# Optimization experiments

Hardware: AMD Instinct MI355X
Metric: run time of the kernel (lower is better)

The kernel has to match this reference:

```python
import jax, jax.numpy as jnp
import numpy as np

LN_EPS = 1e-5

def setup_inputs() -> dict:
    key = jax.random.key(0)
    ks = jax.random.split(key, 7)
    B, S, D = 16, 2048, 512
    scale_g = 1.0 / np.sqrt(2 * D)
    scale_c = 1.0 / np.sqrt(2 * D)
    return {
        "points": jax.random.normal(ks[0], (B, S, D), dtype=jnp.float32),
        "W_gate": jax.random.uniform(ks[1], (2 * D, 2 * D), jnp.float32, -scale_g, scale_g),
        "b_gate": jax.random.uniform(ks[2], (2 * D,), jnp.float32, -scale_g, scale_g),
        "W_cand": jax.random.uniform(ks[3], (2 * D, D), jnp.float32, -scale_c, scale_c),
        "b_cand": jax.random.uniform(ks[4], (D,), jnp.float32, -scale_c, scale_c),
        "gamma": jnp.ones((D,), jnp.float32),
        "beta": jnp.zeros((D,), jnp.float32),
    }

def _layer_norm(x, gamma, beta):
    mu = jnp.mean(x, axis=-1, keepdims=True)
    var = jnp.mean(jnp.square(x - mu), axis=-1, keepdims=True)
    return (x - mu) * jax.lax.rsqrt(var + LN_EPS) * gamma + beta

def reference(points, W_gate, b_gate, W_cand, b_cand, gamma, beta):
    B, S, D = points.shape
    h0 = jnp.zeros((B, D), dtype=points.dtype)

    def step(h, p_t):  # p_t: [B, D]
        combined = jnp.concatenate([p_t, h], axis=1)          # [B, 2D]
        gates = combined @ W_gate + b_gate                    # [B, 2D]
        r = jax.nn.sigmoid(gates[:, :D])
        z = jax.nn.sigmoid(gates[:, D:])
        cand_in = jnp.concatenate([p_t, r * h], axis=1)       # [B, 2D]
        c = jnp.tanh(cand_in @ W_cand + b_cand)               # [B, D]
        h_new = (1.0 - z) * h + z * c
        return h_new, h_new

    _, states = jax.lax.scan(step, h0, jnp.swapaxes(points, 0, 1))  # [S, B, D]
    states = jnp.swapaxes(states, 0, 1)                             # [B, S, D]
    displacement = states - points
    deformed = points + displacement
    return _layer_norm(deformed, gamma, beta)
```

## Files before the change

kernel.cpp:

```cpp
#include <hip/hip_runtime.h>


typedef _Float16 half8 __attribute__((ext_vector_type(8)));
typedef _Float16 half4 __attribute__((ext_vector_type(4)));
typedef float floatx4 __attribute__((ext_vector_type(4)));
typedef int int4v __attribute__((ext_vector_type(4)));

#define NBLK 16
#define TPB 256
#define S_LEN 2048

#define SZ_WPK (96ull * 16 * 64 * 8 * 2)
#define OFF_WHPK 0ull
#define OFF_WXPK (OFF_WHPK + SZ_WPK)
#define OFF_HBUF (OFF_WXPK + SZ_WPK)
#define OFF_RH (OFF_HBUF + 32768ull)
#define OFF_XGT (OFF_RH + 32768ull)

__device__ __forceinline__ float sigmoid_f(float x) {
  return 1.f / (1.f + __expf(-x));
}
__device__ __forceinline__ float tanh_f(float x) {
  x = fminf(15.f, fmaxf(-15.f, x));
  float e = __expf(2.f * x);
  return (e - 1.f) / (e + 1.f);
}

__device__ __forceinline__ void ld8_cg(const unsigned* p, int4v (&d)[8]) {
  asm volatile(
      "global_load_dwordx4 %0, %8, off sc0 sc1\n\t"
      "global_load_dwordx4 %1, %8, off offset:16 sc0 sc1\n\t"
      "global_load_dwordx4 %2, %8, off offset:128 sc0 sc1\n\t"
      "global_load_dwordx4 %3, %8, off offset:144 sc0 sc1\n\t"
      "global_load_dwordx4 %4, %8, off offset:256 sc0 sc1\n\t"
      "global_load_dwordx4 %5, %8, off offset:272 sc0 sc1\n\t"
      "global_load_dwordx4 %6, %8, off offset:384 sc0 sc1\n\t"
      "global_load_dwordx4 %7, %8, off offset:400 sc0 sc1\n\t"
      "s_waitcnt vmcnt(0)"
      : "=&v"(d[0]), "=&v"(d[1]), "=&v"(d[2]), "=&v"(d[3]), "=&v"(d[4]),
        "=&v"(d[5]), "=&v"(d[6]), "=&v"(d[7])
      : "v"(p)
      : "memory");
}
__device__ __forceinline__ void st_dw(unsigned* p, unsigned v) {
  asm volatile("global_store_dword %0, %1, off sc0 sc1" ::"v"(p), "v"(v)
               : "memory");
}
__device__ __forceinline__ unsigned pk2(unsigned p1, unsigned p0) {
  return __builtin_amdgcn_perm(p1, p0, 0x05040100u);
}

__device__ __forceinline__ void stage_val(const unsigned* p, unsigned tokhi,
                                          int4v* lds_dst) {
  int4v d[8];
  for (;;) {
    ld8_cg(p, d);
    unsigned acc = 0;
#pragma unroll
    for (int u = 0; u < 8; ++u)
#pragma unroll
      for (int c = 0; c < 4; ++c) acc |= ((unsigned)d[u][c]) ^ tokhi;
    if (__all((int)((acc >> 16) == 0u))) break;
    __builtin_amdgcn_s_sleep(2);
  }
#pragma unroll
  for (int u = 0; u < 4; ++u) {
    int4v f;
    f[0] = (int)pk2((unsigned)d[2 * u][1], (unsigned)d[2 * u][0]);
    f[1] = (int)pk2((unsigned)d[2 * u][3], (unsigned)d[2 * u][2]);
    f[2] = (int)pk2((unsigned)d[2 * u + 1][1], (unsigned)d[2 * u + 1][0]);
    f[3] = (int)pk2((unsigned)d[2 * u + 1][3], (unsigned)d[2 * u + 1][2]);
    lds_dst[u * 64] = f;
  }
}

__global__ void pack_kernel(const float* __restrict__ Wg,
                            const float* __restrict__ Wc,
                            _Float16* __restrict__ Whpk,
                            _Float16* __restrict__ Wxpk) {
  int unit = blockIdx.x * 4 + (threadIdx.x >> 6);
  int lane = threadIdx.x & 63;
  int set = (unit >= 1536) ? 1 : 0;
  int rem = unit - set * 1536;
  int tile = rem >> 4, kc = rem & 15;
  int kb = kc * 32 + ((lane >> 4) << 3);
  int n = lane & 15;
  int row0 = set ? 0 : 512;
  half8 w;
  if (tile < 64) {
    int col = tile * 16 + n;
#pragma unroll
    for (int jj = 0; jj < 8; ++jj)
      w[jj] = (_Float16)Wg[(size_t)(row0 + kb + jj) * 1024 + col];
  } else {
    int col = (tile - 64) * 16 + n;
#pragma unroll
    for (int jj = 0; jj < 8; ++jj)
      w[jj] = (_Float16)Wc[(size_t)(row0 + kb + jj) * 512 + col];
  }
  _Float16* dst = set ? Wxpk : Whpk;
  *(half8*)(dst + ((size_t)rem * 64 + lane) * 8) = w;
}

__global__ __launch_bounds__(TPB) void xgemm_kernel(
    const float* __restrict__ points, const float* __restrict__ b_gate,
    const float* __restrict__ b_cand, const _Float16* __restrict__ Wxpk,
    _Float16* __restrict__ xgt) {
  __shared__ _Float16 x_lds[16][520];
  const int tid = threadIdx.x;
  const int wave = tid >> 6, lane = tid & 63;
  const int ln15 = lane & 15, q = lane >> 4;
  const int t = blockIdx.x;
  const int m = tid & 15, ch = tid >> 4;

  const float* xp = points + ((size_t)m * S_LEN + t) * 512 + ch * 32;
#pragma unroll
  for (int u = 0; u < 4; ++u) {
    float4 f0 = ((const float4*)xp)[2 * u];
    float4 f1 = ((const float4*)xp)[2 * u + 1];
    half8 hv;
    hv[0] = (_Float16)f0.x; hv[1] = (_Float16)f0.y;
    hv[2] = (_Float16)f0.z; hv[3] = (_Float16)f0.w;
    hv[4] = (_Float16)f1.x; hv[5] = (_Float16)f1.y;
    hv[6] = (_Float16)f1.z; hv[7] = (_Float16)f1.w;
    *(half8*)&x_lds[m][ch * 32 + u * 8] = hv;
  }
  __syncthreads();

  for (int tile = wave; tile < 96; tile += 4) {
    const _Float16* W = Wxpk + (size_t)tile * 8192;
    floatx4 a0 = {0.f, 0.f, 0.f, 0.f}, a1 = {0.f, 0.f, 0.f, 0.f};
#pragma unroll
    for (int kc = 0; kc < 16; kc += 2) {
      a0 = __builtin_amdgcn_mfma_f32_16x16x32_f16(
          *(const half8*)&x_lds[ln15][kc * 32 + q * 8],
          *(const half8*)(W + ((size_t)kc * 64 + lane) * 8), a0, 0, 0, 0);
      a1 = __builtin_amdgcn_mfma_f32_16x16x32_f16(
          *(const half8*)&x_lds[ln15][(kc + 1) * 32 + q * 8],
          *(const half8*)(W + ((size_t)(kc + 1) * 64 + lane) * 8), a1, 0, 0, 0);
    }
    float bias = (tile < 64) ? b_gate[tile * 16 + ln15]
                             : b_cand[(tile - 64) * 16 + ln15];
    half4 o;
#pragma unroll
    for (int i = 0; i < 4; ++i) o[i] = (_Float16)(a0[i] + a1[i] + bias);
    *(half4*)(xgt + (((size_t)t * 96 + tile) * 16 + ln15) * 16 + q * 4) = o;
  }
}

__global__ __launch_bounds__(TPB, 1) void rec_kernel(
    const _Float16* __restrict__ Whpk, const _Float16* __restrict__ xgt,
    unsigned* __restrict__ h2, unsigned* __restrict__ rh2,
    float* __restrict__ out) {
  __shared__ int4v hsh[2][1024];
  __shared__ float z_lds[16][36];

  const int tid = threadIdx.x;
  const int wave = tid >> 6, lane = tid & 63;
  const int ln15 = lane & 15, q = lane >> 4;
  const int j = blockIdx.x;

  const int twA = (wave < 2) ? (2 * j + wave) : (32 + 2 * j + (wave - 2));
  const int twB = 64 + 2 * j + (wave & 1);
  const int colA = 32 * j + 16 * (wave & 1) + ln15;

  half8 wA[16], wB[16];
  {
    const _Float16* sA = Whpk + (size_t)twA * 8192 + lane * 8;
#pragma unroll
    for (int kc = 0; kc < 16; ++kc) wA[kc] = *(const half8*)(sA + kc * 512);
  }
  if (wave < 2) {
    const _Float16* sB = Whpk + (size_t)twB * 8192 + lane * 8;
#pragma unroll
    for (int kc = 0; kc < 16; ++kc) wB[kc] = *(const half8*)(sB + kc * 512);
  }

  const unsigned* h2rd = h2 + ln15 * 512 + q * 8 + wave * 128;
  const unsigned* rh2rd = rh2 + ln15 * 512 + q * 8 + wave * 128;
  unsigned* rh2wr = rh2 + (q * 4) * 512 + colA;
  unsigned* h2wr = h2 + (q * 4) * 512 + colA;
  int4v* ldsA = &hsh[0][(4 * wave) * 64 + lane];
  int4v* ldsB = &hsh[1][(4 * wave) * 64 + lane];

  const _Float16* xga_p = xgt + ((size_t)twA * 16 + ln15) * 16 + q * 4;
  const _Float16* xcb_p = xgt + ((size_t)twB * 16 + ln15) * 16 + q * 4;
  half4 xga = *(const half4*)xga_p;
  half4 xcb = {0, 0, 0, 0};
  if (wave < 2) xcb = *(const half4*)xcb_p;

  float hreg[4] = {0.f, 0.f, 0.f, 0.f};

  for (int t = 0; t < S_LEN; ++t) {
    const size_t pn = (size_t)((t + 1 < S_LEN) ? t + 1 : t) * 24576;
    const unsigned tok1 = (unsigned)t + 1u;
    const unsigned tokhi1 = tok1 << 16;

    stage_val(h2rd, ((unsigned)t) << 16, ldsA);
    __syncthreads();

    floatx4 a0 = {0.f, 0.f, 0.f, 0.f}, a1 = {0.f, 0.f, 0.f, 0.f};
#pragma unroll
    for (int kc = 0; kc < 16; kc += 2) {
      a0 = __builtin_amdgcn_mfma_f32_16x16x32_f16(
          *(const half8*)&hsh[0][kc * 64 + lane], wA[kc], a0, 0, 0, 0);
      a1 = __builtin_amdgcn_mfma_f32_16x16x32_f16(
          *(const half8*)&hsh[0][(kc + 1) * 64 + lane], wA[kc + 1], a1, 0, 0,
          0);
    }
    if (wave < 2) {
      half4 xga_nx = *(const half4*)(xga_p + pn);
#pragma unroll
      for (int i = 0; i < 4; ++i) {
        float r = sigmoid_f(a0[i] + a1[i] + (float)xga[i]);
        unsigned hv = (unsigned)__builtin_bit_cast(unsigned short,
                                                   (_Float16)(r * hreg[i]));
        st_dw(rh2wr + i * 512, tokhi1 | hv);
      }
      xga = xga_nx;
    } else {
#pragma unroll
      for (int i = 0; i < 4; ++i)
        z_lds[q * 4 + i][16 * (wave - 2) + ln15] =
            sigmoid_f(a0[i] + a1[i] + (float)xga[i]);
      xga = *(const half4*)(xga_p + pn);
    }

    stage_val(rh2rd, tokhi1, ldsB);
    __syncthreads();

    if (wave < 2) {
      floatx4 b0 = {0.f, 0.f, 0.f, 0.f}, b1 = {0.f, 0.f, 0.f, 0.f};
#pragma unroll
      for (int kc = 0; kc < 16; kc += 2) {
        b0 = __builtin_amdgcn_mfma_f32_16x16x32_f16(
            *(const half8*)&hsh[1][kc * 64 + lane], wB[kc], b0, 0, 0, 0);
        b1 = __builtin_amdgcn_mfma_f32_16x16x32_f16(
            *(const half8*)&hsh[1][(kc + 1) * 64 + lane], wB[kc + 1], b1, 0, 0,
            0);
      }
      half4 xcb_nx = *(const half4*)(xcb_p + pn);
#pragma unroll
      for (int i = 0; i < 4; ++i) {
        float cv = tanh_f(b0[i] + b1[i] + (float)xcb[i]);
        float zz = z_lds[q * 4 + i][16 * wave + ln15];
        float hn = hreg[i] + zz * (cv - hreg[i]);
        _Float16 hh = (_Float16)hn;
        hreg[i] = (float)hh;
        unsigned hb = (unsigned)__builtin_bit_cast(unsigned short, hh);
        st_dw(h2wr + i * 512, tokhi1 | hb);
        out[((size_t)(q * 4 + i) * S_LEN + t) * 512 + colA] = hn;
      }
      xcb = xcb_nx;
    }
  }
}

__global__ void ln_kernel(float* __restrict__ out, const float* __restrict__ gamma,
                          const float* __restrict__ beta) {
  int gw = (blockIdx.x * blockDim.x + threadIdx.x) >> 6;
  int lane = threadIdx.x & 63;
  int nw = (gridDim.x * blockDim.x) >> 6;
  float4 ga = ((const float4*)(gamma + lane * 8))[0];
  float4 gb = ((const float4*)(gamma + lane * 8))[1];
  float4 ba = ((const float4*)(beta + lane * 8))[0];
  float4 bb = ((const float4*)(beta + lane * 8))[1];
  for (int r = gw; r < 16 * S_LEN; r += nw) {
    float* p = out + (size_t)r * 512 + lane * 8;
    float4 v0 = ((float4*)p)[0], v1 = ((float4*)p)[1];
    float s = v0.x + v0.y + v0.z + v0.w + v1.x + v1.y + v1.z + v1.w;
    float sq = v0.x * v0.x + v0.y * v0.y + v0.z * v0.z + v0.w * v0.w +
               v1.x * v1.x + v1.y * v1.y + v1.z * v1.z + v1.w * v1.w;
#pragma unroll
    for (int off = 32; off > 0; off >>= 1) {
      s += __shfl_xor(s, off);
      sq += __shfl_xor(sq, off);
    }
    float mean = s * (1.f / 512.f);
    float var = sq * (1.f / 512.f) - mean * mean;
    float rstd = rsqrtf(var + 1e-5f);
    v0.x = (v0.x - mean) * rstd * ga.x + ba.x;
    v0.y = (v0.y - mean) * rstd * ga.y + ba.y;
    v0.z = (v0.z - mean) * rstd * ga.z + ba.z;
    v0.w = (v0.w - mean) * rstd * ga.w + ba.w;
    v1.x = (v1.x - mean) * rstd * gb.x + bb.x;
    v1.y = (v1.y - mean) * rstd * gb.y + bb.y;
    v1.z = (v1.z - mean) * rstd * gb.z + bb.z;
    v1.w = (v1.w - mean) * rstd * gb.w + bb.w;
    ((float4*)p)[0] = v0;
    ((float4*)p)[1] = v1;
  }
}

extern "C" void kernel_launch(void* const* d_in, const int* in_sizes, int n_in,
                              void* d_out, int out_size, void* d_ws,
                              size_t ws_size, hipStream_t stream) {
  const float* points = (const float*)d_in[0];
  const float* W_gate = (const float*)d_in[1];
  const float* b_gate = (const float*)d_in[2];
  const float* W_cand = (const float*)d_in[3];
  const float* b_cand = (const float*)d_in[4];
  const float* gamma = (const float*)d_in[5];
  const float* beta = (const float*)d_in[6];
  char* ws = (char*)d_ws;
  _Float16* Whpk = (_Float16*)(ws + OFF_WHPK);
  _Float16* Wxpk = (_Float16*)(ws + OFF_WXPK);
  unsigned* h2 = (unsigned*)(ws + OFF_HBUF);
  unsigned* rh2 = (unsigned*)(ws + OFF_RH);
  _Float16* xgt = (_Float16*)(ws + OFF_XGT);
  float* out = (float*)d_out;

  hipMemsetAsync(ws + OFF_HBUF, 0, 65536, stream);
  pack_kernel<<<768, 256, 0, stream>>>(W_gate, W_cand, Whpk, Wxpk);
  xgemm_kernel<<<S_LEN, TPB, 0, stream>>>(points, b_gate, b_cand, Wxpk, xgt);
  rec_kernel<<<NBLK, TPB, 0, stream>>>(Whpk, xgt, h2, rh2, out);
  ln_kernel<<<512, 256, 0, stream>>>(out, gamma, beta);
}
```

Baseline: 12.59 ms.

## Co-locate recurrent blocks on one XCC and use device-scope-free coherence

Launches 128 blocks, reads each block's XCC id, and elects 16 blocks that share one XCC to run the recurrence while the others exit. A handshake test checks whether loads and stores with only the sc0 cache bit stay coherent among the elected blocks. If the test passes, the per-step h/rh exchange skips the sc1 system-scope bit and the sleep in the polling loop, cutting inter-block sync latency through the shared L2. This adds startup election overhead and depends on enough blocks landing on a single XCC. It falls back to the old sc1 path if the test fails.

```diff
diff --git a/kernel.cpp b/kernel.cpp
--- a/kernel.cpp
+++ b/kernel.cpp
@@ -7,6 +7,7 @@
 typedef int int4v __attribute__((ext_vector_type(4)));
 
 #define NBLK 16
+#define NGRID 128
 #define TPB 256
 #define S_LEN 2048
 
@@ -15,7 +16,8 @@
 #define OFF_WXPK (OFF_WHPK + SZ_WPK)
 #define OFF_HBUF (OFF_WXPK + SZ_WPK)
 #define OFF_RH (OFF_HBUF + 32768ull)
-#define OFF_XGT (OFF_RH + 32768ull)
+#define OFF_CNT (OFF_RH + 32768ull)
+#define OFF_XGT (OFF_CNT + 16384ull)
 
 __device__ __forceinline__ float sigmoid_f(float x) {
   return 1.f / (1.f + __expf(-x));
@@ -26,42 +28,81 @@
   return (e - 1.f) / (e + 1.f);
 }
 
-__device__ __forceinline__ void ld8_cg(const unsigned* p, int4v (&d)[8]) {
-  asm volatile(
-      "global_load_dwordx4 %0, %8, off sc0 sc1\n\t"
-      "global_load_dwordx4 %1, %8, off offset:16 sc0 sc1\n\t"
-      "global_load_dwordx4 %2, %8, off offset:128 sc0 sc1\n\t"
-      "global_load_dwordx4 %3, %8, off offset:144 sc0 sc1\n\t"
-      "global_load_dwordx4 %4, %8, off offset:256 sc0 sc1\n\t"
-      "global_load_dwordx4 %5, %8, off offset:272 sc0 sc1\n\t"
-      "global_load_dwordx4 %6, %8, off offset:384 sc0 sc1\n\t"
-      "global_load_dwordx4 %7, %8, off offset:400 sc0 sc1\n\t"
-      "s_waitcnt vmcnt(0)"
-      : "=&v"(d[0]), "=&v"(d[1]), "=&v"(d[2]), "=&v"(d[3]), "=&v"(d[4]),
-        "=&v"(d[5]), "=&v"(d[6]), "=&v"(d[7])
-      : "v"(p)
-      : "memory");
-}
-__device__ __forceinline__ void st_dw(unsigned* p, unsigned v) {
-  asm volatile("global_store_dword %0, %1, off sc0 sc1" ::"v"(p), "v"(v)
-               : "memory");
+template <int SC1>
+__device__ __forceinline__ void ld8_t(const unsigned* p, int4v (&d)[8]) {
+  if constexpr (SC1) {
+    asm volatile(
+        "global_load_dwordx4 %0, %8, off sc0 sc1\n\t"
+        "global_load_dwordx4 %1, %8, off offset:16 sc0 sc1\n\t"
+        "global_load_dwordx4 %2, %8, off offset:128 sc0 sc1\n\t"
+        "global_load_dwordx4 %3, %8, off offset:144 sc0 sc1\n\t"
+        "global_load_dwordx4 %4, %8, off offset:256 sc0 sc1\n\t"
+        "global_load_dwordx4 %5, %8, off offset:272 sc0 sc1\n\t"
+        "global_load_dwordx4 %6, %8, off offset:384 sc0 sc1\n\t"
+        "global_load_dwordx4 %7, %8, off offset:400 sc0 sc1\n\t"
+        "s_waitcnt vmcnt(0)"
+        : "=&v"(d[0]), "=&v"(d[1]), "=&v"(d[2]), "=&v"(d[3]), "=&v"(d[4]),
+          "=&v"(d[5]), "=&v"(d[6]), "=&v"(d[7])
+        : "v"(p)
+        : "memory");
+  } else {
+    asm volatile(
+        "global_load_dwordx4 %0, %8, off sc0\n\t"
+        "global_load_dwordx4 %1, %8, off offset:16 sc0\n\t"
+        "global_load_dwordx4 %2, %8, off offset:128 sc0\n\t"
+        "global_load_dwordx4 %3, %8, off offset:144 sc0\n\t"
+        "global_load_dwordx4 %4, %8, off offset:256 sc0\n\t"
+        "global_load_dwordx4 %5, %8, off offset:272 sc0\n\t"
+        "global_load_dwordx4 %6, %8, off offset:384 sc0\n\t"
+        "global_load_dwordx4 %7, %8, off offset:400 sc0\n\t"
+        "s_waitcnt vmcnt(0)"
+        : "=&v"(d[0]), "=&v"(d[1]), "=&v"(d[2]), "=&v"(d[3]), "=&v"(d[4]),
+          "=&v"(d[5]), "=&v"(d[6]), "=&v"(d[7])
+        : "v"(p)
+        : "memory");
+  }
+}
+template <int SC1>
+__device__ __forceinline__ void st_dw_t(unsigned* p, unsigned v) {
+  if constexpr (SC1)
+    asm volatile("global_store_dword %0, %1, off sc0 sc1" ::"v"(p), "v"(v)
+                 : "memory");
+  else
+    asm volatile("global_store_dword %0, %1, off sc0" ::"v"(p), "v"(v)
+                 : "memory");
+}
+template <int SC1>
+__device__ __forceinline__ unsigned ld_dw_t(const unsigned* p) {
+  unsigned v;
+  if constexpr (SC1)
+    asm volatile("global_load_dword %0, %1, off sc0 sc1\n\ts_waitcnt vmcnt(0)"
+                 : "=v"(v)
+                 : "v"(p)
+                 : "memory");
+  else
+    asm volatile("global_load_dword %0, %1, off sc0\n\ts_waitcnt vmcnt(0)"
+                 : "=v"(v)
+                 : "v"(p)
+                 : "memory");
+  return v;
 }
 __device__ __forceinline__ unsigned pk2(unsigned p1, unsigned p0) {
   return __builtin_amdgcn_perm(p1, p0, 0x05040100u);
 }
 
-__device__ __forceinline__ void stage_val(const unsigned* p, unsigned tokhi,
-                                          int4v* lds_dst) {
+template <int SC1>
+__device__ __forceinline__ void stage_val_t(const unsigned* p, unsigned tokhi,
+                                            int4v* lds_dst) {
   int4v d[8];
   for (;;) {
-    ld8_cg(p, d);
+    ld8_t<SC1>(p, d);
     unsigned acc = 0;
 #pragma unroll
     for (int u = 0; u < 8; ++u)
 #pragma unroll
       for (int c = 0; c < 4; ++c) acc |= ((unsigned)d[u][c]) ^ tokhi;
     if (__all((int)((acc >> 16) == 0u))) break;
-    __builtin_amdgcn_s_sleep(2);
+    if constexpr (SC1) __builtin_amdgcn_s_sleep(2);
   }
 #pragma unroll
   for (int u = 0; u < 4; ++u) {
@@ -148,17 +189,14 @@
   }
 }
 
-__global__ __launch_bounds__(TPB, 1) void rec_kernel(
-    const _Float16* __restrict__ Whpk, const _Float16* __restrict__ xgt,
-    unsigned* __restrict__ h2, unsigned* __restrict__ rh2,
-    float* __restrict__ out) {
-  __shared__ int4v hsh[2][1024];
-  __shared__ float z_lds[16][36];
-
-  const int tid = threadIdx.x;
-  const int wave = tid >> 6, lane = tid & 63;
+template <int SC1>
+__device__ void scan_loop(int j, int wave, int lane,
+                          const _Float16* __restrict__ Whpk,
+                          const _Float16* __restrict__ xgt,
+                          unsigned* __restrict__ h2,
+                          unsigned* __restrict__ rh2, float* __restrict__ out,
+                          int4v (*hsh)[1024], float (*z_lds)[36]) {
   const int ln15 = lane & 15, q = lane >> 4;
-  const int j = blockIdx.x;
 
   const int twA = (wave < 2) ? (2 * j + wave) : (32 + 2 * j + (wave - 2));
   const int twB = 64 + 2 * j + (wave & 1);
@@ -196,7 +234,7 @@
     const unsigned tok1 = (unsigned)t + 1u;
     const unsigned tokhi1 = tok1 << 16;
 
-    stage_val(h2rd, ((unsigned)t) << 16, ldsA);
+    stage_val_t<SC1>(h2rd, ((unsigned)t) << 16, ldsA);
     __syncthreads();
 
     floatx4 a0 = {0.f, 0.f, 0.f, 0.f}, a1 = {0.f, 0.f, 0.f, 0.f};
@@ -215,7 +253,7 @@
         float r = sigmoid_f(a0[i] + a1[i] + (float)xga[i]);
         unsigned hv = (unsigned)__builtin_bit_cast(unsigned short,
                                                    (_Float16)(r * hreg[i]));
-        st_dw(rh2wr + i * 512, tokhi1 | hv);
+        st_dw_t<SC1>(rh2wr + i * 512, tokhi1 | hv);
       }
       xga = xga_nx;
     } else {
@@ -226,7 +264,7 @@
       xga = *(const half4*)(xga_p + pn);
     }
 
-    stage_val(rh2rd, tokhi1, ldsB);
+    stage_val_t<SC1>(rh2rd, tokhi1, ldsB);
     __syncthreads();
 
     if (wave < 2) {
@@ -248,12 +286,85 @@
         _Float16 hh = (_Float16)hn;
         hreg[i] = (float)hh;
         unsigned hb = (unsigned)__builtin_bit_cast(unsigned short, hh);
-        st_dw(h2wr + i * 512, tokhi1 | hb);
+        st_dw_t<SC1>(h2wr + i * 512, tokhi1 | hb);
         out[((size_t)(q * 4 + i) * S_LEN + t) * 512 + colA] = hn;
       }
       xcb = xcb_nx;
     }
   }
+}
+
+__global__ __launch_bounds__(TPB, 1) void rec_kernel(
+    const _Float16* __restrict__ Whpk, const _Float16* __restrict__ xgt,
+    unsigned* __restrict__ h2, unsigned* __restrict__ rh2,
+    unsigned* __restrict__ cnt, float* __restrict__ out) {
+  __shared__ int4v hsh[2][1024];
+  __shared__ float z_lds[16][36];
+  __shared__ int s_j, s_fast;
+
+  const int tid = threadIdx.x;
+  const int wave = tid >> 6, lane = tid & 63;
+  const int bid = blockIdx.x;
+
+  if (tid == 0) {
+    unsigned x;
+    asm volatile("s_getreg_b32 %0, hwreg(HW_REG_XCC_ID)" : "=s"(x));
+    st_dw_t<1>(cnt + bid, 0x100u | (x & 7u));
+  }
+  if (wave == 0) {
+    unsigned a, b;
+    for (;;) {
+      a = ld_dw_t<1>(cnt + lane);
+      b = ld_dw_t<1>(cnt + 64 + lane);
+      if (__all((int)((a != 0u) && (b != 0u)))) break;
+      __builtin_amdgcn_s_sleep(2);
+    }
+    unsigned xa = a & 7u, xb = b & 7u;
+    int win = 0;
+    for (int x = 0; x < 8; ++x) {
+      int c = __popcll(__ballot(xa == (unsigned)x)) +
+              __popcll(__ballot(xb == (unsigned)x));
+      if (c >= NBLK) { win = x; break; }
+    }
+    unsigned myx = (bid < 64) ? __shfl(xa, bid) : __shfl(xb, bid - 64);
+    int rank = __popcll(__ballot(xa == (unsigned)win && lane < bid)) +
+               __popcll(__ballot(xb == (unsigned)win && (64 + lane) < bid));
+    int isw = (myx == (unsigned)win && rank < NBLK) ? 1 : 0;
+    int fast = 0;
+    if (isw) {
+      int ok = 1;
+      for (int r = 0; r < 4 && ok; ++r) {
+        if (rank == r && lane == 0) st_dw_t<0>(cnt + 192, 1000u + (unsigned)r);
+        unsigned v = 0;
+        for (int it = 0; it < 1000; ++it) {
+          v = ld_dw_t<0>(cnt + 192);
+          if (v == 1000u + (unsigned)r) break;
+          __builtin_amdgcn_s_sleep(1);
+        }
+        if (!__all((int)(v == 1000u + (unsigned)r))) ok = 0;
+      }
+      if (lane == 0) st_dw_t<1>(cnt + 160 + rank, ok ? 2u : 1u);
+      unsigned rv;
+      for (;;) {
+        rv = (lane < NBLK) ? ld_dw_t<1>(cnt + 160 + lane) : 2u;
+        if (__all((int)(rv != 0u))) break;
+        __builtin_amdgcn_s_sleep(2);
+      }
+      fast = __all((int)(rv == 2u)) ? 1 : 0;
+    }
+    if (lane == 0) {
+      s_j = isw ? rank : -1;
+      s_fast = fast;
+    }
+  }
+  __syncthreads();
+  const int j = s_j;
+  if (j < 0) return;
+
+  if (s_fast)
+    scan_loop<0>(j, wave, lane, Whpk, xgt, h2, rh2, out, hsh, z_lds);
+  else
+    scan_loop<1>(j, wave, lane, Whpk, xgt, h2, rh2, out, hsh, z_lds);
 }
 
 __global__ void ln_kernel(float* __restrict__ out, const float* __restrict__ gamma,
@@ -307,12 +418,13 @@
   _Float16* Wxpk = (_Float16*)(ws + OFF_WXPK);
   unsigned* h2 = (unsigned*)(ws + OFF_HBUF);
   unsigned* rh2 = (unsigned*)(ws + OFF_RH);
+  unsigned* cnt = (unsigned*)(ws + OFF_CNT);
   _Float16* xgt = (_Float16*)(ws + OFF_XGT);
   float* out = (float*)d_out;
 
-  hipMemsetAsync(ws + OFF_HBUF, 0, 65536, stream);
+  hipMemsetAsync(ws + OFF_HBUF, 0, 81920, stream);
   pack_kernel<<<768, 256, 0, stream>>>(W_gate, W_cand, Whpk, Wxpk);
   xgemm_kernel<<<S_LEN, TPB, 0, stream>>>(points, b_gate, b_cand, Wxpk, xgt);
-  rec_kernel<<<NBLK, TPB, 0, stream>>>(Whpk, xgt, h2, rh2, out);
+  rec_kernel<<<NGRID, TPB, 0, stream>>>(Whpk, xgt, h2, rh2, cnt, out);
   ln_kernel<<<512, 256, 0, stream>>>(out, gamma, beta);
 }
```

Measured after the change: 14.16 ms. 1.12x slower.
